# Optimization experiments

Hardware: AMD Instinct MI355X
Metric: run time of the kernel (lower is better)

## Reference

```python
import jax, jax.numpy as jnp
import numpy as np

N_NODES = 100000


def _graph_conv(x, W, b, src, dst, norm):
    # DGL GraphConv(norm='left'): scale source features by 1/out_degree,
    # aggregate (sum over incoming edges). in_feats > out_feats so weight
    # multiply happens before aggregation (mathematically equivalent either way).
    h = x @ W  # [N, out]
    msg = (h * norm[:, None])[src]  # gather per-edge messages [E, out]
    agg = jax.ops.segment_sum(msg, dst, num_segments=N_NODES)
    return agg + b


def setup_inputs() -> dict:
    key = jax.random.key(0)
    ks = jax.random.split(key, 10)
    in_f, hid_f, out_f = 256, 128, 64
    n_edges = 1_600_000
    feat = jax.random.normal(ks[0], (N_NODES, in_f), dtype=jnp.float32)
    src = jax.random.randint(ks[1], (n_edges,), 0, N_NODES, dtype=jnp.int32)
    dst = jax.random.randint(ks[2], (n_edges,), 0, N_NODES, dtype=jnp.int32)
    noise = jax.random.normal(ks[3], (N_NODES, out_f), dtype=jnp.float32)
    s1 = 1.0 / np.sqrt(in_f)
    s2 = 1.0 / np.sqrt(hid_f)
    W_shared = jax.random.uniform(ks[4], (in_f, hid_f), minval=-s1, maxval=s1, dtype=jnp.float32)
    b_shared = jnp.zeros((hid_f,), jnp.float32)
    W_mu = jax.random.uniform(ks[5], (hid_f, out_f), minval=-s2, maxval=s2, dtype=jnp.float32)
    b_mu = jnp.zeros((out_f,), jnp.float32)
    W_ls = jax.random.uniform(ks[6], (hid_f, out_f), minval=-s2, maxval=s2, dtype=jnp.float32)
    b_ls = jnp.zeros((out_f,), jnp.float32)
    return {"feat": feat, "W_shared": W_shared, "b_shared": b_shared,
            "W_mu": W_mu, "b_mu": b_mu, "W_ls": W_ls, "b_ls": b_ls,
            "noise": noise, "src": src, "dst": dst}


def reference(feat, W_shared, b_shared, W_mu, b_mu, W_ls, b_ls, noise, src, dst):
    # left-norm: 1 / out_degree (clamped to >= 1, as DGL does)
    deg_out = jax.ops.segment_sum(jnp.ones_like(src, jnp.float32), src,
                                  num_segments=N_NODES)
    norm = 1.0 / jnp.maximum(deg_out, 1.0)
    # shared first GraphConv with ReLU activation
    h = jax.nn.relu(_graph_conv(feat, W_shared, b_shared, src, dst, norm))
    # two heads (no activation)
    mu = _graph_conv(h, W_mu, b_mu, src, dst, norm)
    log_sigma = _graph_conv(h, W_ls, b_ls, src, dst, norm)
    # reparameterized sample
    return mu + noise * jnp.exp(log_sigma)
```

## Files before the change

kernel.cpp:

```cpp
#include <hip/hip_runtime.h>
#include <hip/hip_bf16.h>
#include <math.h>

typedef __attribute__((ext_vector_type(8))) short short8;
typedef __attribute__((ext_vector_type(4))) float f32x4;

__device__ __forceinline__ unsigned short f2bf(float f) {
    unsigned int u = __float_as_uint(f);
    u += 0x7FFF + ((u >> 16) & 1);
    return (unsigned short)(u >> 16);
}
__device__ __forceinline__ float b2f(unsigned short s) {
    return __uint_as_float(((unsigned int)s) << 16);
}
__device__ __forceinline__ unsigned int f2bf2(float a, float b) {
    __hip_bfloat162 h = __float22bfloat162_rn(make_float2(a, b));
    return *(unsigned int*)&h;
}
__device__ __forceinline__ void gl_lds16(const void* g, void* l) {
    __builtin_amdgcn_global_load_lds(
        (const __attribute__((address_space(1))) void*)g,
        (__attribute__((address_space(3))) void*)l, 16, 0, 0);
}

#define EB 2048
#define SH 9
#define BSZ 512
#define CAP 10240

__global__ __launch_bounds__(256)
void k12_scatter(const int* __restrict__ src, const int* __restrict__ dst,
                 int* __restrict__ gcnt, int* __restrict__ parr,
                 unsigned short* __restrict__ sarr, int E, int NB) {
    __shared__ int se[EB];
    __shared__ int sdn[EB];
    __shared__ int ssn[EB];
    __shared__ int histd[256], hists[256];
    int t = threadIdx.x;
    histd[t] = 0; hists[t] = 0;
    __syncthreads();
    int base = blockIdx.x * EB;
    int end = min(base + EB, E);
    for (int e = base + 4 * t; e < end; e += 1024) {
        if (e + 3 < end) {
            int4 s4 = *(const int4*)&src[e];
            int4 d4 = *(const int4*)&dst[e];
            int li = e - base;
#pragma unroll
            for (int j = 0; j < 4; ++j) {
                int sv = (j == 0) ? s4.x : (j == 1) ? s4.y : (j == 2) ? s4.z : s4.w;
                int dv = (j == 0) ? d4.x : (j == 1) ? d4.y : (j == 2) ? d4.z : d4.w;
                int db = dv >> SH, sb = sv >> SH;
                int ds = atomicAdd(&histd[db], 1);
                int ss = atomicAdd(&hists[sb], 1);
                se[li + j] = (sv << SH) | (dv & (BSZ - 1));
                sdn[li + j] = (db << 16) | ds;
                ssn[li + j] = (sb << 16) | ss;
            }
        } else {
            for (int q = e; q < end; ++q) {
                int sv = src[q], dv = dst[q];
                int li = q - base;
                int db = dv >> SH, sb = sv >> SH;
                int ds = atomicAdd(&histd[db], 1);
                int ss = atomicAdd(&hists[sb], 1);
                se[li] = (sv << SH) | (dv & (BSZ - 1));
                sdn[li] = (db << 16) | ds;
                ssn[li] = (sb << 16) | ss;
            }
        }
    }
    __syncthreads();
    for (int i = t; i < NB; i += 256) {
        int h = histd[i];
        histd[i] = h ? atomicAdd(&gcnt[i], h) : 0;
        int h2 = hists[i];
        hists[i] = h2 ? atomicAdd(&gcnt[NB + i], h2) : 0;
    }
    __syncthreads();
    for (int e = base + 4 * t; e < end; e += 1024) {
        int m = min(4, end - e);
        for (int j = 0; j < m; ++j) {
            int li = e - base + j;
            int pe = se[li];
            int a = sdn[li];
            int db = a >> 16, ds = a & 0xffff;
            int off = histd[db] + ds;
            if (off < CAP) parr[(size_t)db * CAP + off] = pe;
            int b2 = ssn[li];
            int sb = b2 >> 16, ss = b2 & 0xffff;
            int offs = hists[sb] + ss;
            if (offs < CAP) sarr[(size_t)sb * CAP + offs] = (unsigned short)((pe >> SH) & (BSZ - 1));
        }
    }
}

__global__ __launch_bounds__(1024)
void k3_both(const int* __restrict__ parr, const unsigned short* __restrict__ sarr,
             const int* __restrict__ gcnt, int2* __restrict__ rowse,
             int* __restrict__ col, float* __restrict__ norm, int N, int NB) {
    __shared__ int hist[512], sc[512];
    int b = blockIdx.x, t = threadIdx.x;
    if (b < NB) {
        int ne = min(gcnt[b], CAP);
        int ebase = b * CAP;
        if (t < 512) hist[t] = 0;
        __syncthreads();
        for (int i = t; i < ne; i += 1024)
            atomicAdd(&hist[parr[ebase + i] & (BSZ - 1)], 1);
        __syncthreads();
        int h = 0;
        if (t < 512) { h = hist[t]; sc[t] = h; }
        __syncthreads();
        for (int off = 1; off < 512; off <<= 1) {
            int u = (t < 512 && t >= off) ? sc[t - off] : 0;
            __syncthreads();
            if (t < 512) sc[t] += u;
            __syncthreads();
        }
        if (t < 512) {
            int excl = sc[t] - h;
            int node = b * BSZ + t;
            if (node < N) rowse[node] = make_int2(ebase + excl, ebase + excl + h);
            hist[t] = ebase + excl;
        }
        __syncthreads();
        for (int i = t; i < ne; i += 1024) {
            int pr = parr[ebase + i];
            int slot = atomicAdd(&hist[pr & (BSZ - 1)], 1);
            col[slot] = pr >> SH;
        }
    } else {
        int bs = b - NB;
        int ne = min(gcnt[NB + bs], CAP);
        int sbase = bs * CAP;
        if (t < 512) hist[t] = 0;
        __syncthreads();
        for (int i = t; i < ne; i += 1024)
            atomicAdd(&hist[sarr[sbase + i]], 1);
        __syncthreads();
        int node = bs * BSZ + t;
        if (t < 512 && node < N) {
            int d = hist[t];
            norm[node] = 1.0f / (float)(d > 1 ? d : 1);
        }
    }
}


__global__ __launch_bounds__(256)
void k_wprep(const float* __restrict__ Wsh, const float* __restrict__ Wmu,
             const float* __restrict__ Wls, unsigned short* __restrict__ W1T,
             unsigned short* __restrict__ W2T, int* __restrict__ gcnt) {
    int b = blockIdx.x, t = threadIdx.x;
    if (b == 0) {
        gcnt[t] = 0; gcnt[256 + t] = 0; gcnt[512 + t] = 0; gcnt[768 + t] = 0;
    }
    if (b < 128) {
        W1T[(size_t)b * 256 + t] = f2bf(Wsh[(size_t)t * 128 + b]);
    } else {
        int n = b - 128;
        if (t < 128) {
            float v = (n < 64) ? Wmu[(size_t)t * 64 + n]
                               : Wls[(size_t)t * 64 + (n - 64)];
            W2T[(size_t)n * 128 + t] = f2bf(v);
        }
    }
}

__global__ __launch_bounds__(256)
void k_gemm1(const float* __restrict__ A, int M,
             const unsigned short* __restrict__ W1T,
             const float* __restrict__ norm, unsigned short* __restrict__ outb) {
    __shared__ char ldsA[64 * 1040];
    const int w = threadIdx.x >> 6;
    const int lane = threadIdx.x & 63;
    const int quad = lane >> 4;
    const int l16 = lane & 15;
    const int cl = w * 16 + l16;
    const int r0 = blockIdx.x * 64;

#pragma unroll
    for (int i = 0; i < 16; ++i) {
        int row = r0 + w * 16 + i;
        if (row >= M) row = M - 1;
        const char* g = (const char*)A + (size_t)row * 1024 + lane * 16;
        char* l = ldsA + (w * 16 + i) * 1040 + lane * 16;
        gl_lds16(g, l);
    }

    short8 bw[2][8];
#pragma unroll
    for (int hf = 0; hf < 2; ++hf) {
        const unsigned short* wp = W1T + (size_t)(hf * 64 + cl) * 256 + quad * 8;
#pragma unroll
        for (int ks = 0; ks < 8; ++ks)
            bw[hf][ks] = *(const short8*)(wp + ks * 32);
    }
    __syncthreads();

    f32x4 acc[4][2];
#pragma unroll
    for (int m = 0; m < 4; ++m) {
        acc[m][0] = (f32x4){0.f, 0.f, 0.f, 0.f};
        acc[m][1] = (f32x4){0.f, 0.f, 0.f, 0.f};
    }
#pragma unroll
    for (int ks = 0; ks < 8; ++ks) {
#pragma unroll
        for (int m = 0; m < 4; ++m) {
            const float* pr = (const float*)(ldsA + (m * 16 + l16) * 1040 +
                                             (ks * 32 + quad * 8) * 4);
            float4 x = *(const float4*)pr;
            float4 y = *(const float4*)(pr + 4);
            union { short8 v; unsigned int u[4]; } c;
            c.u[0] = f2bf2(x.x, x.y);
            c.u[1] = f2bf2(x.z, x.w);
            c.u[2] = f2bf2(y.x, y.y);
            c.u[3] = f2bf2(y.z, y.w);
            acc[m][0] = __builtin_amdgcn_mfma_f32_16x16x32_bf16(bw[0][ks], c.v, acc[m][0], 0, 0, 0);
            acc[m][1] = __builtin_amdgcn_mfma_f32_16x16x32_bf16(bw[1][ks], c.v, acc[m][1], 0, 0, 0);
        }
    }
    const int colbase = w * 16 + quad * 4;
#pragma unroll
    for (int m = 0; m < 4; ++m) {
        int row = r0 + m * 16 + l16;
        if (row < M) {
            float nm = norm[row];
            ushort4 o0, o1;
            o0.x = f2bf(acc[m][0][0] * nm); o0.y = f2bf(acc[m][0][1] * nm);
            o0.z = f2bf(acc[m][0][2] * nm); o0.w = f2bf(acc[m][0][3] * nm);
            o1.x = f2bf(acc[m][1][0] * nm); o1.y = f2bf(acc[m][1][1] * nm);
            o1.z = f2bf(acc[m][1][2] * nm); o1.w = f2bf(acc[m][1][3] * nm);
            *(ushort4*)&outb[(size_t)row * 128 + colbase] = o0;
            *(ushort4*)&outb[(size_t)row * 128 + 64 + colbase] = o1;
        }
    }
}

__device__ __forceinline__ float4 gather_row(int e0, int e1,
                                             const int* __restrict__ col,
                                             const ushort4* __restrict__ base, int l) {
    float4 acc = make_float4(0.f, 0.f, 0.f, 0.f);
    int e = e0;
    for (; e + 7 < e1; e += 8) {
        ushort4 v0 = base[(size_t)col[e] * 32 + l];
        ushort4 v1 = base[(size_t)col[e + 1] * 32 + l];
        ushort4 v2 = base[(size_t)col[e + 2] * 32 + l];
        ushort4 v3 = base[(size_t)col[e + 3] * 32 + l];
        ushort4 v4 = base[(size_t)col[e + 4] * 32 + l];
        ushort4 v5 = base[(size_t)col[e + 5] * 32 + l];
        ushort4 v6 = base[(size_t)col[e + 6] * 32 + l];
        ushort4 v7 = base[(size_t)col[e + 7] * 32 + l];
        acc.x += ((b2f(v0.x) + b2f(v1.x)) + (b2f(v2.x) + b2f(v3.x))) +
                 ((b2f(v4.x) + b2f(v5.x)) + (b2f(v6.x) + b2f(v7.x)));
        acc.y += ((b2f(v0.y) + b2f(v1.y)) + (b2f(v2.y) + b2f(v3.y))) +
                 ((b2f(v4.y) + b2f(v5.y)) + (b2f(v6.y) + b2f(v7.y)));
        acc.z += ((b2f(v0.z) + b2f(v1.z)) + (b2f(v2.z) + b2f(v3.z))) +
                 ((b2f(v4.z) + b2f(v5.z)) + (b2f(v6.z) + b2f(v7.z)));
        acc.w += ((b2f(v0.w) + b2f(v1.w)) + (b2f(v2.w) + b2f(v3.w))) +
                 ((b2f(v4.w) + b2f(v5.w)) + (b2f(v6.w) + b2f(v7.w)));
    }
    for (; e + 1 < e1; e += 2) {
        ushort4 a = base[(size_t)col[e] * 32 + l];
        ushort4 b = base[(size_t)col[e + 1] * 32 + l];
        acc.x += b2f(a.x) + b2f(b.x);
        acc.y += b2f(a.y) + b2f(b.y);
        acc.z += b2f(a.z) + b2f(b.z);
        acc.w += b2f(a.w) + b2f(b.w);
    }
    if (e < e1) {
        ushort4 a = base[(size_t)col[e] * 32 + l];
        acc.x += b2f(a.x); acc.y += b2f(a.y); acc.z += b2f(a.z); acc.w += b2f(a.w);
    }
    return acc;
}

__global__ __launch_bounds__(256)
void k_spmm_relu(const int2* __restrict__ rowse, const int* __restrict__ col,
                 const unsigned short* __restrict__ hxb, const float* __restrict__ bias,
                 const float* __restrict__ norm, unsigned short* __restrict__ hb, int N) {
    int g = (blockIdx.x * blockDim.x + threadIdx.x) >> 5;
    int l = threadIdx.x & 31;
    if (g >= N) return;
    int2 se = rowse[g];
    float4 acc = gather_row(se.x, se.y, col, (const ushort4*)hxb, l);
    float4 bi = ((const float4*)bias)[l];
    float nm = norm[g];
    ushort4 r;
    r.x = f2bf(fmaxf(acc.x + bi.x, 0.f) * nm);
    r.y = f2bf(fmaxf(acc.y + bi.y, 0.f) * nm);
    r.z = f2bf(fmaxf(acc.z + bi.z, 0.f) * nm);
    r.w = f2bf(fmaxf(acc.w + bi.w, 0.f) * nm);
    ((ushort4*)hb)[(size_t)g * 32 + l] = r;
}

__global__ __launch_bounds__(256)
void k_spmm_gemm_out(const int2* __restrict__ rowse, const int* __restrict__ col,
                     const unsigned short* __restrict__ hnb,
                     const unsigned short* __restrict__ W2T,
                     const float* __restrict__ bmu, const float* __restrict__ bls,
                     const float* __restrict__ noise, float* __restrict__ out, int N) {
    __shared__ char ldsB[8 * 1040];
    __shared__ int wq;
    const int tid = threadIdx.x;
    const int r0 = blockIdx.x * 32;
    if (tid == 0) wq = 0;
    const int lane = tid & 63;
    const int w = tid >> 6;
    const int quad = lane >> 4;
    const int l16 = lane & 15;
    const int cl = w * 16 + l16;
    short8 bw[2][4];
#pragma unroll
    for (int hf = 0; hf < 2; ++hf) {
        const unsigned short* wp = W2T + (size_t)(hf * 64 + cl) * 128 + quad * 8;
#pragma unroll
        for (int ks = 0; ks < 4; ++ks)
            bw[hf][ks] = *(const short8*)(wp + ks * 32);
    }
    __syncthreads();
    const int l = tid & 31;
    const ushort4* base = (const ushort4*)hnb;
    for (;;) {
        int lrow;
        if (l == 0) lrow = atomicAdd(&wq, 1);
        lrow = __shfl(lrow, lane & 32, 64);
        if (lrow >= 32) break;
        int g = r0 + lrow;
        float4 acc = make_float4(0.f, 0.f, 0.f, 0.f);
        if (g < N) {
            int2 se2 = rowse[g];
            acc = gather_row(se2.x, se2.y, col, base, l);
        }
        ushort4 r;
        r.x = f2bf(acc.x); r.y = f2bf(acc.y); r.z = f2bf(acc.z); r.w = f2bf(acc.w);
        *(ushort4*)(ldsB + (lrow >> 2) * 1040 + (lrow & 3) * 256 + l * 8) = r;
    }
    __syncthreads();
    f32x4 acc2[2][2];
#pragma unroll
    for (int mi = 0; mi < 2; ++mi) {
        acc2[mi][0] = (f32x4){0.f, 0.f, 0.f, 0.f};
        acc2[mi][1] = (f32x4){0.f, 0.f, 0.f, 0.f};
    }
#pragma unroll
    for (int ks = 0; ks < 4; ++ks) {
#pragma unroll
        for (int mi = 0; mi < 2; ++mi) {
            int row = mi * 16 + l16;
            short8 af = *(const short8*)(ldsB + (row >> 2) * 1040 + (row & 3) * 256 +
                                         (ks * 32 + quad * 8) * 2);
            acc2[mi][0] = __builtin_amdgcn_mfma_f32_16x16x32_bf16(bw[0][ks], af, acc2[mi][0], 0, 0, 0);
            acc2[mi][1] = __builtin_amdgcn_mfma_f32_16x16x32_bf16(bw[1][ks], af, acc2[mi][1], 0, 0, 0);
        }
    }
    const int colbase = w * 16 + quad * 4;
    float4 bm = ((const float4*)bmu)[colbase >> 2];
    float4 bl = ((const float4*)bls)[colbase >> 2];
#pragma unroll
    for (int mi = 0; mi < 2; ++mi) {
        int row = r0 + mi * 16 + l16;
        if (row < N) {
            float4 nz = ((const float4*)noise)[(size_t)row * 16 + (colbase >> 2)];
            float4 o;
            o.x = (acc2[mi][0][0] + bm.x) + nz.x * expf(acc2[mi][1][0] + bl.x);
            o.y = (acc2[mi][0][1] + bm.y) + nz.y * expf(acc2[mi][1][1] + bl.y);
            o.z = (acc2[mi][0][2] + bm.z) + nz.z * expf(acc2[mi][1][2] + bl.z);
            o.w = (acc2[mi][0][3] + bm.w) + nz.w * expf(acc2[mi][1][3] + bl.w);
            ((float4*)out)[(size_t)row * 16 + (colbase >> 2)] = o;
        }
    }
}

__global__ __launch_bounds__(256)
void k_gemm2(const unsigned short* __restrict__ A, int M,
             const unsigned short* __restrict__ W2T,
             unsigned short* __restrict__ outb) {
    __shared__ char ldsB[16 * 1040];
    const int w = threadIdx.x >> 6;
    const int lane = threadIdx.x & 63;
    const int quad = lane >> 4;
    const int l16 = lane & 15;
    const int cl = w * 16 + l16;
    const int r0 = blockIdx.x * 64;
#pragma unroll
    for (int i = 0; i < 4; ++i) {
        int c = w * 4 + i;
        int crow = r0 + c * 4;
        if (crow + 4 > M) crow = M - 4;
        const char* g = (const char*)A + (size_t)crow * 256 + lane * 16;
        char* l = ldsB + c * 1040 + lane * 16;
        gl_lds16(g, l);
    }
    short8 bw[2][4];
#pragma unroll
    for (int hf = 0; hf < 2; ++hf) {
        const unsigned short* wp = W2T + (size_t)(hf * 64 + cl) * 128 + quad * 8;
#pragma unroll
        for (int ks = 0; ks < 4; ++ks)
            bw[hf][ks] = *(const short8*)(wp + ks * 32);
    }
    __syncthreads();
    f32x4 acc[4][2];
#pragma unroll
    for (int m = 0; m < 4; ++m) {
        acc[m][0] = (f32x4){0.f, 0.f, 0.f, 0.f};
        acc[m][1] = (f32x4){0.f, 0.f, 0.f, 0.f};
    }
#pragma unroll
    for (int ks = 0; ks < 4; ++ks) {
#pragma unroll
        for (int m = 0; m < 4; ++m) {
            int row = m * 16 + l16;
            short8 af = *(const short8*)(ldsB + (row >> 2) * 1040 + (row & 3) * 256 +
                                         (ks * 32 + quad * 8) * 2);
            acc[m][0] = __builtin_amdgcn_mfma_f32_16x16x32_bf16(bw[0][ks], af, acc[m][0], 0, 0, 0);
            acc[m][1] = __builtin_amdgcn_mfma_f32_16x16x32_bf16(bw[1][ks], af, acc[m][1], 0, 0, 0);
        }
    }
    const int colbase = w * 16 + quad * 4;
#pragma unroll
    for (int m = 0; m < 4; ++m) {
        int row = r0 + m * 16 + l16;
        if (row < M) {
            ushort4 o0, o1;
            o0.x = f2bf(acc[m][0][0]); o0.y = f2bf(acc[m][0][1]);
            o0.z = f2bf(acc[m][0][2]); o0.w = f2bf(acc[m][0][3]);
            o1.x = f2bf(acc[m][1][0]); o1.y = f2bf(acc[m][1][1]);
            o1.z = f2bf(acc[m][1][2]); o1.w = f2bf(acc[m][1][3]);
            *(ushort4*)&outb[(size_t)row * 128 + colbase] = o0;
            *(ushort4*)&outb[(size_t)row * 128 + 64 + colbase] = o1;
        }
    }
}

__global__ __launch_bounds__(256)
void k_spmm_out(const int2* __restrict__ rowse, const int* __restrict__ col,
                const unsigned short* __restrict__ hcb, const float* __restrict__ bmu,
                const float* __restrict__ bls, const float* __restrict__ noise,
                float* __restrict__ out, int N) {
    int g = (blockIdx.x * blockDim.x + threadIdx.x) >> 5;
    int l = threadIdx.x & 31;
    if (g >= N) return;
    int2 se = rowse[g];
    float4 acc = gather_row(se.x, se.y, col, (const ushort4*)hcb, l);
    int lane64 = threadIdx.x & 63;
    int p = (lane64 + 16) & 63;
    float lx = __shfl(acc.x, p, 64);
    float ly = __shfl(acc.y, p, 64);
    float lz = __shfl(acc.z, p, 64);
    float lw = __shfl(acc.w, p, 64);
    if (l < 16) {
        float4 bm = ((const float4*)bmu)[l];
        float4 bl = ((const float4*)bls)[l];
        float4 nz = ((const float4*)noise)[(size_t)g * 16 + l];
        float4 o;
        o.x = (acc.x + bm.x) + nz.x * expf(lx + bl.x);
        o.y = (acc.y + bm.y) + nz.y * expf(ly + bl.y);
        o.z = (acc.z + bm.z) + nz.z * expf(lz + bl.z);
        o.w = (acc.w + bm.w) + nz.w * expf(lw + bl.w);
        ((float4*)out)[(size_t)g * 16 + l] = o;
    }
}

static inline char* align64(char* p) {
    return (char*)(((uintptr_t)p + 63) & ~(uintptr_t)63);
}

extern "C" void kernel_launch(void* const* d_in, const int* in_sizes, int n_in,
                              void* d_out, int out_size, void* d_ws, size_t ws_size,
                              hipStream_t stream) {
    const float* feat  = (const float*)d_in[0];
    const float* Wsh   = (const float*)d_in[1];
    const float* bsh   = (const float*)d_in[2];
    const float* Wmu   = (const float*)d_in[3];
    const float* bmu   = (const float*)d_in[4];
    const float* Wls   = (const float*)d_in[5];
    const float* bls   = (const float*)d_in[6];
    const float* noise = (const float*)d_in[7];
    const int*   src   = (const int*)d_in[8];
    const int*   dst   = (const int*)d_in[9];
    float* out = (float*)d_out;

    const int N = in_sizes[0] / 256;
    const int E = in_sizes[8];
    const int PB = (E + EB - 1) / EB;
    const int NB = (N + BSZ - 1) / BSZ;
    const int NB2 = 2 * NB;

    char* p = (char*)d_ws;
    float* norm   = (float*)p;                  p += (size_t)N * 4;          p = align64(p);
    int2* rowse   = (int2*)p;                   p += (size_t)N * 8;          p = align64(p);
    int* gcnt     = (int*)p;                    p += 1024 * 4;               p = align64(p);
    unsigned short* W1T = (unsigned short*)p;   p += (size_t)128 * 256 * 2;
    unsigned short* W2T = (unsigned short*)p;   p += (size_t)128 * 128 * 2;
    p = align64(p);
    int* parr     = (int*)p;                    p += (size_t)NB * CAP * 4;
    unsigned short* sarr = (unsigned short*)p;  p += (size_t)NB * CAP * 2;   p = align64(p);
    int* col      = (int*)p;                    p += (size_t)NB * CAP * 4;   p = align64(p);
    unsigned short* hxb = (unsigned short*)p;   p += (size_t)N * 128 * 2;    p = align64(p);
    unsigned short* hnb = (unsigned short*)p;
    size_t need_fused = (size_t)((p + (size_t)N * 128 * 2) - (char*)d_ws);
    bool fused = (need_fused <= ws_size);

    k_wprep<<<256, 256, 0, stream>>>(Wsh, Wmu, Wls, W1T, W2T, gcnt);
    k12_scatter<<<PB, 256, 0, stream>>>(src, dst, gcnt, parr, sarr, E, NB);
    k3_both<<<NB2, 1024, 0, stream>>>(parr, sarr, gcnt, rowse, col, norm, N, NB);

    int gtiles = (N + 63) / 64;
    k_gemm1<<<gtiles, 256, 0, stream>>>(feat, N, W1T, norm, hxb);
    if (fused) {
        k_spmm_relu<<<(N * 32 + 255) / 256, 256, 0, stream>>>(rowse, col, hxb, bsh, norm, hnb, N);
        k_spmm_gemm_out<<<(N + 31) / 32, 256, 0, stream>>>(rowse, col, hnb, W2T, bmu, bls, noise, out, N);
    } else {
        unsigned short* hb = (unsigned short*)d_out;
        k_spmm_relu<<<(N * 32 + 255) / 256, 256, 0, stream>>>(rowse, col, hxb, bsh, norm, hb, N);
        k_gemm2<<<gtiles, 256, 0, stream>>>(hb, N, W2T, hxb);
        k_spmm_out<<<(N * 32 + 255) / 256, 256, 0, stream>>>(rowse, col, hxb, bmu, bls, noise, out, N);
    }
}
```

Before: 416.0 us.

## Replace fused gather-GEMM output kernel with separate GEMM2 then gather path

Removes the fused k_spmm_gemm_out path, which gathered and aggregated the 128-wide hidden features per row and then ran the output GEMM. It is replaced by an unconditional three-step path: ReLU aggregation, a dense GEMM2 that applies the out-degree normalisation in its epilogue, and a final gather over the 128-wide combined mu/log_sigma features. The norm multiply moves from the first SpMM epilogue into GEMM2, which is valid because the norm is a per-row scale. This avoids the per-block atomic row queue and LDS staging of the fused kernel, at the cost of an extra kernel launch and an extra pass writing and reading the hidden activations.

```diff
diff --git a/kernel.cpp b/kernel.cpp
--- a/kernel.cpp
+++ b/kernel.cpp
@@ -220,6 +220,72 @@
             c.u[3] = f2bf2(y.z, y.w);
             acc[m][0] = __builtin_amdgcn_mfma_f32_16x16x32_bf16(bw[0][ks], c.v, acc[m][0], 0, 0, 0);
             acc[m][1] = __builtin_amdgcn_mfma_f32_16x16x32_bf16(bw[1][ks], c.v, acc[m][1], 0, 0, 0);
+        }
+    }
+    const int colbase = w * 16 + quad * 4;
+#pragma unroll
+    for (int m = 0; m < 4; ++m) {
+        int row = r0 + m * 16 + l16;
+        if (row < M) {
+            float nm = norm[row];
+            ushort4 o0, o1;
+            o0.x = f2bf(acc[m][0][0] * nm); o0.y = f2bf(acc[m][0][1] * nm);
+            o0.z = f2bf(acc[m][0][2] * nm); o0.w = f2bf(acc[m][0][3] * nm);
+            o1.x = f2bf(acc[m][1][0] * nm); o1.y = f2bf(acc[m][1][1] * nm);
+            o1.z = f2bf(acc[m][1][2] * nm); o1.w = f2bf(acc[m][1][3] * nm);
+            *(ushort4*)&outb[(size_t)row * 128 + colbase] = o0;
+            *(ushort4*)&outb[(size_t)row * 128 + 64 + colbase] = o1;
+        }
+    }
+}
+
+__global__ __launch_bounds__(256)
+void k_gemm2(const unsigned short* __restrict__ A, int M,
+             const unsigned short* __restrict__ W2T,
+             const float* __restrict__ norm, unsigned short* __restrict__ outb) {
+    __shared__ char ldsB[16 * 1040];
+    const int w = threadIdx.x >> 6;
+    const int lane = threadIdx.x & 63;
+    const int quad = lane >> 4;
+    const int l16 = lane & 15;
+    const int cl = w * 16 + l16;
+    const int r0 = blockIdx.x * 64;
+
+#pragma unroll
+    for (int i = 0; i < 4; ++i) {
+        int c = w * 4 + i;
+        int crow = r0 + c * 4;
+        if (crow + 4 > M) crow = M - 4;
+        const char* g = (const char*)A + (size_t)crow * 256 + lane * 16;
+        char* l = ldsB + c * 1040 + lane * 16;
+        gl_lds16(g, l);
+    }
+
+    short8 bw[2][4];
+#pragma unroll
+    for (int hf = 0; hf < 2; ++hf) {
+        const unsigned short* wp = W2T + (size_t)(hf * 64 + cl) * 128 + quad * 8;
+#pragma unroll
+        for (int ks = 0; ks < 4; ++ks)
+            bw[hf][ks] = *(const short8*)(wp + ks * 32);
+    }
+    __syncthreads();
+
+    f32x4 acc[4][2];
+#pragma unroll
+    for (int m = 0; m < 4; ++m) {
+        acc[m][0] = (f32x4){0.f, 0.f, 0.f, 0.f};
+        acc[m][1] = (f32x4){0.f, 0.f, 0.f, 0.f};
+    }
+#pragma unroll
+    for (int ks = 0; ks < 4; ++ks) {
+#pragma unroll
+        for (int m = 0; m < 4; ++m) {
+            int row = m * 16 + l16;
+            short8 af = *(const short8*)(ldsB + (row >> 2) * 1040 + (row & 3) * 256 +
+                                         (ks * 32 + quad * 8) * 2);
+            acc[m][0] = __builtin_amdgcn_mfma_f32_16x16x32_bf16(bw[0][ks], af, acc[m][0], 0, 0, 0);
+            acc[m][1] = __builtin_amdgcn_mfma_f32_16x16x32_bf16(bw[1][ks], af, acc[m][1], 0, 0, 0);
         }
     }
     const int colbase = w * 16 + quad * 4;
@@ -280,160 +346,19 @@
 __global__ __launch_bounds__(256)
 void k_spmm_relu(const int2* __restrict__ rowse, const int* __restrict__ col,
                  const unsigned short* __restrict__ hxb, const float* __restrict__ bias,
-                 const float* __restrict__ norm, unsigned short* __restrict__ hb, int N) {
+                 unsigned short* __restrict__ hb, int N) {
     int g = (blockIdx.x * blockDim.x + threadIdx.x) >> 5;
     int l = threadIdx.x & 31;
     if (g >= N) return;
     int2 se = rowse[g];
     float4 acc = gather_row(se.x, se.y, col, (const ushort4*)hxb, l);
     float4 bi = ((const float4*)bias)[l];
-    float nm = norm[g];
     ushort4 r;
-    r.x = f2bf(fmaxf(acc.x + bi.x, 0.f) * nm);
-    r.y = f2bf(fmaxf(acc.y + bi.y, 0.f) * nm);
-    r.z = f2bf(fmaxf(acc.z + bi.z, 0.f) * nm);
-    r.w = f2bf(fmaxf(acc.w + bi.w, 0.f) * nm);
+    r.x = f2bf(fmaxf(acc.x + bi.x, 0.f));
+    r.y = f2bf(fmaxf(acc.y + bi.y, 0.f));
+    r.z = f2bf(fmaxf(acc.z + bi.z, 0.f));
+    r.w = f2bf(fmaxf(acc.w + bi.w, 0.f));
     ((ushort4*)hb)[(size_t)g * 32 + l] = r;
-}
-
-__global__ __launch_bounds__(256)
-void k_spmm_gemm_out(const int2* __restrict__ rowse, const int* __restrict__ col,
-                     const unsigned short* __restrict__ hnb,
-                     const unsigned short* __restrict__ W2T,
-                     const float* __restrict__ bmu, const float* __restrict__ bls,
-                     const float* __restrict__ noise, float* __restrict__ out, int N) {
-    __shared__ char ldsB[8 * 1040];
-    __shared__ int wq;
-    const int tid = threadIdx.x;
-    const int r0 = blockIdx.x * 32;
-    if (tid == 0) wq = 0;
-    const int lane = tid & 63;
-    const int w = tid >> 6;
-    const int quad = lane >> 4;
-    const int l16 = lane & 15;
-    const int cl = w * 16 + l16;
-    short8 bw[2][4];
-#pragma unroll
-    for (int hf = 0; hf < 2; ++hf) {
-        const unsigned short* wp = W2T + (size_t)(hf * 64 + cl) * 128 + quad * 8;
-#pragma unroll
-        for (int ks = 0; ks < 4; ++ks)
-            bw[hf][ks] = *(const short8*)(wp + ks * 32);
-    }
-    __syncthreads();
-    const int l = tid & 31;
-    const ushort4* base = (const ushort4*)hnb;
-    for (;;) {
-        int lrow;
-        if (l == 0) lrow = atomicAdd(&wq, 1);
-        lrow = __shfl(lrow, lane & 32, 64);
-        if (lrow >= 32) break;
-        int g = r0 + lrow;
-        float4 acc = make_float4(0.f, 0.f, 0.f, 0.f);
-        if (g < N) {
-            int2 se2 = rowse[g];
-            acc = gather_row(se2.x, se2.y, col, base, l);
-        }
-        ushort4 r;
-        r.x = f2bf(acc.x); r.y = f2bf(acc.y); r.z = f2bf(acc.z); r.w = f2bf(acc.w);
-        *(ushort4*)(ldsB + (lrow >> 2) * 1040 + (lrow & 3) * 256 + l * 8) = r;
-    }
-    __syncthreads();
-    f32x4 acc2[2][2];
-#pragma unroll
-    for (int mi = 0; mi < 2; ++mi) {
-        acc2[mi][0] = (f32x4){0.f, 0.f, 0.f, 0.f};
-        acc2[mi][1] = (f32x4){0.f, 0.f, 0.f, 0.f};
-    }
-#pragma unroll
-    for (int ks = 0; ks < 4; ++ks) {
-#pragma unroll
-        for (int mi = 0; mi < 2; ++mi) {
-            int row = mi * 16 + l16;
-            short8 af = *(const short8*)(ldsB + (row >> 2) * 1040 + (row & 3) * 256 +
-                                         (ks * 32 + quad * 8) * 2);
-            acc2[mi][0] = __builtin_amdgcn_mfma_f32_16x16x32_bf16(bw[0][ks], af, acc2[mi][0], 0, 0, 0);
-            acc2[mi][1] = __builtin_amdgcn_mfma_f32_16x16x32_bf16(bw[1][ks], af, acc2[mi][1], 0, 0, 0);
-        }
-    }
-    const int colbase = w * 16 + quad * 4;
-    float4 bm = ((const float4*)bmu)[colbase >> 2];
-    float4 bl = ((const float4*)bls)[colbase >> 2];
-#pragma unroll
-    for (int mi = 0; mi < 2; ++mi) {
-        int row = r0 + mi * 16 + l16;
-        if (row < N) {
-            float4 nz = ((const float4*)noise)[(size_t)row * 16 + (colbase >> 2)];
-            float4 o;
-            o.x = (acc2[mi][0][0] + bm.x) + nz.x * expf(acc2[mi][1][0] + bl.x);
-            o.y = (acc2[mi][0][1] + bm.y) + nz.y * expf(acc2[mi][1][1] + bl.y);
-            o.z = (acc2[mi][0][2] + bm.z) + nz.z * expf(acc2[mi][1][2] + bl.z);
-            o.w = (acc2[mi][0][3] + bm.w) + nz.w * expf(acc2[mi][1][3] + bl.w);
-            ((float4*)out)[(size_t)row * 16 + (colbase >> 2)] = o;
-        }
-    }
-}
-
-__global__ __launch_bounds__(256)
-void k_gemm2(const unsigned short* __restrict__ A, int M,
-             const unsigned short* __restrict__ W2T,
-             unsigned short* __restrict__ outb) {
-    __shared__ char ldsB[16 * 1040];
-    const int w = threadIdx.x >> 6;
-    const int lane = threadIdx.x & 63;
-    const int quad = lane >> 4;
-    const int l16 = lane & 15;
-    const int cl = w * 16 + l16;
-    const int r0 = blockIdx.x * 64;
-#pragma unroll
-    for (int i = 0; i < 4; ++i) {
-        int c = w * 4 + i;
-        int crow = r0 + c * 4;
-        if (crow + 4 > M) crow = M - 4;
-        const char* g = (const char*)A + (size_t)crow * 256 + lane * 16;
-        char* l = ldsB + c * 1040 + lane * 16;
-        gl_lds16(g, l);
-    }
-    short8 bw[2][4];
-#pragma unroll
-    for (int hf = 0; hf < 2; ++hf) {
-        const unsigned short* wp = W2T + (size_t)(hf * 64 + cl) * 128 + quad * 8;
-#pragma unroll
-        for (int ks = 0; ks < 4; ++ks)
-            bw[hf][ks] = *(const short8*)(wp + ks * 32);
-    }
-    __syncthreads();
-    f32x4 acc[4][2];
-#pragma unroll
-    for (int m = 0; m < 4; ++m) {
-        acc[m][0] = (f32x4){0.f, 0.f, 0.f, 0.f};
-        acc[m][1] = (f32x4){0.f, 0.f, 0.f, 0.f};
-    }
-#pragma unroll
-    for (int ks = 0; ks < 4; ++ks) {
-#pragma unroll
-        for (int m = 0; m < 4; ++m) {
-            int row = m * 16 + l16;
-            short8 af = *(const short8*)(ldsB + (row >> 2) * 1040 + (row & 3) * 256 +
-                                         (ks * 32 + quad * 8) * 2);
-            acc[m][0] = __builtin_amdgcn_mfma_f32_16x16x32_bf16(bw[0][ks], af, acc[m][0], 0, 0, 0);
-            acc[m][1] = __builtin_amdgcn_mfma_f32_16x16x32_bf16(bw[1][ks], af, acc[m][1], 0, 0, 0);
-        }
-    }
-    const int colbase = w * 16 + quad * 4;
-#pragma unroll
-    for (int m = 0; m < 4; ++m) {
-        int row = r0 + m * 16 + l16;
-        if (row < M) {
-            ushort4 o0, o1;
-            o0.x = f2bf(acc[m][0][0]); o0.y = f2bf(acc[m][0][1]);
-            o0.z = f2bf(acc[m][0][2]); o0.w = f2bf(acc[m][0][3]);
-            o1.x = f2bf(acc[m][1][0]); o1.y = f2bf(acc[m][1][1]);
-            o1.z = f2bf(acc[m][1][2]); o1.w = f2bf(acc[m][1][3]);
-            *(ushort4*)&outb[(size_t)row * 128 + colbase] = o0;
-            *(ushort4*)&outb[(size_t)row * 128 + 64 + colbase] = o1;
-        }
-    }
 }
 
 __global__ __launch_bounds__(256)
@@ -500,10 +425,8 @@
     int* parr     = (int*)p;                    p += (size_t)NB * CAP * 4;
     unsigned short* sarr = (unsigned short*)p;  p += (size_t)NB * CAP * 2;   p = align64(p);
     int* col      = (int*)p;                    p += (size_t)NB * CAP * 4;   p = align64(p);
-    unsigned short* hxb = (unsigned short*)p;   p += (size_t)N * 128 * 2;    p = align64(p);
-    unsigned short* hnb = (unsigned short*)p;
-    size_t need_fused = (size_t)((p + (size_t)N * 128 * 2) - (char*)d_ws);
-    bool fused = (need_fused <= ws_size);
+    unsigned short* hxb = (unsigned short*)p;
+    unsigned short* hb  = (unsigned short*)d_out;
 
     k_wprep<<<256, 256, 0, stream>>>(Wsh, Wmu, Wls, W1T, W2T, gcnt);
     k12_scatter<<<PB, 256, 0, stream>>>(src, dst, gcnt, parr, sarr, E, NB);
@@ -511,13 +434,7 @@
 
     int gtiles = (N + 63) / 64;
     k_gemm1<<<gtiles, 256, 0, stream>>>(feat, N, W1T, norm, hxb);
-    if (fused) {
-        k_spmm_relu<<<(N * 32 + 255) / 256, 256, 0, stream>>>(rowse, col, hxb, bsh, norm, hnb, N);
-        k_spmm_gemm_out<<<(N + 31) / 32, 256, 0, stream>>>(rowse, col, hnb, W2T, bmu, bls, noise, out, N);
-    } else {
-        unsigned short* hb = (unsigned short*)d_out;
-        k_spmm_relu<<<(N * 32 + 255) / 256, 256, 0, stream>>>(rowse, col, hxb, bsh, norm, hb, N);
-        k_gemm2<<<gtiles, 256, 0, stream>>>(hb, N, W2T, hxb);
-        k_spmm_out<<<(N * 32 + 255) / 256, 256, 0, stream>>>(rowse, col, hxb, bmu, bls, noise, out, N);
-    }
-}
+    k_spmm_relu<<<(N * 32 + 255) / 256, 256, 0, stream>>>(rowse, col, hxb, bsh, hb, N);
+    k_gemm2<<<gtiles, 256, 0, stream>>>(hb, N, W2T, norm, hxb);
+    k_spmm_out<<<(N * 32 + 255) / 256, 256, 0, stream>>>(rowse, col, hxb, bmu, bls, noise, out, N);
+}
```

After: 398.5 us. 1.04x faster.
